# Performance work log

Measured on AMD Instinct MI355X. Metric: run time of the kernel, lower is better.

The kernel has to match this reference:

```python
import jax, jax.numpy as jnp
import numpy as np

D_MODEL = 512
N_HEADS = 8
D_K = D_MODEL // N_HEADS
LN_EPS = 1e-5


def setup_inputs() -> dict:
    key = jax.random.key(0)
    ks = jax.random.split(key, 12)
    B, S = 2, 2048
    sc = 1.0 / np.sqrt(D_MODEL)
    inp = {
        'q': jax.random.normal(ks[0], (B, S, D_MODEL), jnp.float32),
        'k': jax.random.normal(ks[1], (B, S, D_MODEL), jnp.float32),
        'v': jax.random.normal(ks[2], (B, S, D_MODEL), jnp.float32),
        'Wq': jax.random.normal(ks[3], (D_MODEL, D_MODEL), jnp.float32) * sc,
        'bq': jnp.zeros((D_MODEL,), jnp.float32),
        'Wk': jax.random.normal(ks[4], (D_MODEL, D_MODEL), jnp.float32) * sc,
        'bk': jnp.zeros((D_MODEL,), jnp.float32),
        'Wv': jax.random.normal(ks[5], (D_MODEL, D_MODEL), jnp.float32) * sc,
        'bv': jnp.zeros((D_MODEL,), jnp.float32),
        'Wo': jax.random.normal(ks[6], (D_MODEL, D_MODEL), jnp.float32) * sc,
        'bo': jnp.zeros((D_MODEL,), jnp.float32),
        'gamma': jnp.ones((D_MODEL,), jnp.float32),
        'beta': jnp.zeros((D_MODEL,), jnp.float32),
    }
    return inp


def _split_heads(x):
    B, S, _ = x.shape
    return x.reshape(B, S, N_HEADS, D_K).transpose(0, 2, 1, 3)  # [B,H,S,d_k]


def reference(q, k, v, Wq, bq, Wk, bk, Wv, bv, Wo, bo, gamma, beta):
    B, S, _ = q.shape
    Q = _split_heads(q @ Wq.T + bq)
    K = _split_heads(k @ Wk.T + bk)
    V = _split_heads(v @ Wv.T + bv)
    scores = jnp.einsum('bhqd,bhkd->bhqk', Q, K) / jnp.sqrt(jnp.float32(D_K))
    attn = jax.nn.softmax(scores, axis=-1)  # [B,H,S,S]
    out = jnp.einsum('bhqk,bhkd->bhqd', attn, V)
    out = out.transpose(0, 2, 1, 3).reshape(B, S, D_MODEL)
    out = out @ Wo.T + bo
    x = out + q  # residual
    mu = jnp.mean(x, axis=-1, keepdims=True)
    var = jnp.mean(jnp.square(x - mu), axis=-1, keepdims=True)
    y = (x - mu) * jax.lax.rsqrt(var + LN_EPS) * gamma + beta
    return (y, attn)
```

## Files before the change

### kernel.cpp

```cpp
#include <hip/hip_runtime.h>
#include <hip/hip_bf16.h>

typedef __attribute__((ext_vector_type(8))) short short8;
typedef __attribute__((ext_vector_type(4))) short short4v;
typedef __attribute__((ext_vector_type(4))) float f32x4;

#define MFMA16(A, B, C) __builtin_amdgcn_mfma_f32_16x16x32_bf16(A, B, C, 0, 0, 0)

#define SEQ 2048
#define DM 512
#define NH 8
#define DK 64
#define NROWS 4096
#define DSPLIT 4
#define ASPLIT 4
#define NT_D (SEQ / DSPLIT / 64)
#define NT_A (SEQ / ASPLIT / 64)
#define C1 0.180336880f

__device__ __forceinline__ short f2bf(float f) {
  union { float f; unsigned u; } x; x.f = f;
  unsigned r = (x.u + 0x7fffu + ((x.u >> 16) & 1u)) >> 16;
  return (short)r;
}
__device__ __forceinline__ float bf2f(short s) {
  union { unsigned u; float f; } x; x.u = ((unsigned)(unsigned short)s) << 16;
  return x.f;
}

__global__ __launch_bounds__(256) void cast_all_kernel(
    const float* __restrict__ q, const float* __restrict__ k, const float* __restrict__ v,
    const float* __restrict__ Wq, const float* __restrict__ Wk,
    const float* __restrict__ Wv, const float* __restrict__ Wo,
    short* __restrict__ qb, short* __restrict__ kb, short* __restrict__ vb,
    short* __restrict__ Wqb, short* __restrict__ Wkb,
    short* __restrict__ Wvb, short* __restrict__ Wob)
{
  int z = blockIdx.z;
  if (z >= 3 && blockIdx.x >= 128) return;
  const float* src;
  short* dst;
  switch (z) {
    case 0: src = q;  dst = qb;  break;
    case 1: src = k;  dst = kb;  break;
    case 2: src = v;  dst = vb;  break;
    case 3: src = Wq; dst = Wqb; break;
    case 4: src = Wk; dst = Wkb; break;
    case 5: src = Wv; dst = Wvb; break;
    default: src = Wo; dst = Wob; break;
  }
  size_t i = ((size_t)blockIdx.x * 256 + threadIdx.x) * 8;
  float4 f0 = *(const float4*)(src + i);
  float4 f1 = *(const float4*)(src + i + 4);
  short8 s;
  s[0] = f2bf(f0.x); s[1] = f2bf(f0.y); s[2] = f2bf(f0.z); s[3] = f2bf(f0.w);
  s[4] = f2bf(f1.x); s[5] = f2bf(f1.y); s[6] = f2bf(f1.z); s[7] = f2bf(f1.w);
  *(short8*)(dst + i) = s;
}

__global__ __launch_bounds__(256) void qkv_proj_kernel(
    const short* __restrict__ qbf, const short* __restrict__ kbf, const short* __restrict__ vbf,
    const short* __restrict__ Wqb, const short* __restrict__ Wkb, const short* __restrict__ Wvb,
    const float* __restrict__ bq, const float* __restrict__ bk, const float* __restrict__ bv,
    short* __restrict__ Qb, short* __restrict__ Kb, short* __restrict__ Vtb)
{
  int z = blockIdx.z;
  const short* X    = (z == 0) ? qbf : (z == 1) ? kbf : vbf;
  const short* W    = (z == 0) ? Wqb : (z == 1) ? Wkb : Wvb;
  const float* bias = (z == 0) ? bq  : (z == 1) ? bk  : bv;

  __shared__ short As[64][40];
  __shared__ short Bs[64][40];

  int t = threadIdx.x;
  int lane = t & 63, wave = t >> 6;
  int wr = wave >> 1, wc = wave & 1;
  int fr = lane & 15, fg = lane >> 4;
  int m0 = blockIdx.x * 64, n0 = blockIdx.y * 64;
  int lrow = t >> 2, lcol = (t & 3) * 8;

  f32x4 acc[2][2] = {};

  short8 a_pf = *(const short8*)(X + (size_t)(m0 + lrow) * DM + lcol);
  short8 b_pf = *(const short8*)(W + (size_t)(n0 + lrow) * DM + lcol);

  for (int k0 = 0; k0 < DM; k0 += 32) {
    __syncthreads();
    *(short8*)&As[lrow][lcol] = a_pf;
    *(short8*)&Bs[lrow][lcol] = b_pf;
    __syncthreads();
    if (k0 + 32 < DM) {
      a_pf = *(const short8*)(X + (size_t)(m0 + lrow) * DM + k0 + 32 + lcol);
      b_pf = *(const short8*)(W + (size_t)(n0 + lrow) * DM + k0 + 32 + lcol);
    }
    short8 a0 = *(const short8*)&As[wr * 32 + fr][fg * 8];
    short8 a1 = *(const short8*)&As[wr * 32 + 16 + fr][fg * 8];
    short8 b0 = *(const short8*)&Bs[wc * 32 + fr][fg * 8];
    short8 b1 = *(const short8*)&Bs[wc * 32 + 16 + fr][fg * 8];
    acc[0][0] = MFMA16(a0, b0, acc[0][0]);
    acc[0][1] = MFMA16(a0, b1, acc[0][1]);
    acc[1][0] = MFMA16(a1, b0, acc[1][0]);
    acc[1][1] = MFMA16(a1, b1, acc[1][1]);
  }

#pragma unroll
  for (int mi = 0; mi < 2; mi++)
#pragma unroll
    for (int ni = 0; ni < 2; ni++)
#pragma unroll
      for (int r = 0; r < 4; r++) {
        int row = m0 + wr * 32 + mi * 16 + fg * 4 + r;
        int col = n0 + wc * 32 + ni * 16 + fr;
        float val = acc[mi][ni][r] + bias[col];
        int bb = row >> 11, s = row & 2047, h = col >> 6, dk = col & 63;
        short o = f2bf(val);
        if (z == 0)      Qb[((size_t)(bb * NH + h) * SEQ + s) * DK + dk] = o;
        else if (z == 1) Kb[((size_t)(bb * NH + h) * SEQ + s) * DK + dk] = o;
        else             Vtb[((size_t)(bb * NH + h) * DK + dk) * SEQ + s] = o;
      }
}

__global__ __launch_bounds__(256) void den_kernel(
    const short* __restrict__ Q, const short* __restrict__ K, float* __restrict__ dp)
{
  __shared__ short Ks[64][72];

  int t = threadIdx.x, lane = t & 63, wave = t >> 6;
  int fr = lane & 15, fg = lane >> 4;
  int bh = blockIdx.y, z = blockIdx.z;
  const short* Qh = Q + (size_t)bh * SEQ * DK;
  const short* Kh = K + (size_t)bh * SEQ * DK;
  int q0 = blockIdx.x * 64 + wave * 16;
  const int kbase = z * (SEQ / DSPLIT);

  short8 qa0 = *(const short8*)(Qh + (q0 + fr) * DK + fg * 8);
  short8 qa1 = *(const short8*)(Qh + (q0 + fr) * DK + 32 + fg * 8);

  int r_st = t >> 2, c_st = (t & 3) * 16;

  const short* kp0 = Kh + (size_t)(kbase + r_st) * DK + c_st;
  short8 k_pf0 = *(const short8*)kp0;
  short8 k_pf1 = *(const short8*)(kp0 + 8);

  float esum = 0.f;

  for (int kt = 0; kt < NT_D; kt++) {
    __syncthreads();
    *(short8*)&Ks[r_st][c_st]     = k_pf0;
    *(short8*)&Ks[r_st][c_st + 8] = k_pf1;
    __syncthreads();
    if (kt + 1 < NT_D) {
      const short* kp = Kh + (size_t)(kbase + (kt + 1) * 64 + r_st) * DK + c_st;
      k_pf0 = *(const short8*)kp;
      k_pf1 = *(const short8*)(kp + 8);
    }
#pragma unroll
    for (int ct = 0; ct < 4; ct++) {
      short8 k0v = *(const short8*)&Ks[ct * 16 + fr][fg * 8];
      short8 k1v = *(const short8*)&Ks[ct * 16 + fr][32 + fg * 8];
      f32x4 zz = {0.f, 0.f, 0.f, 0.f};
      zz = MFMA16(k0v, qa0, zz);
      zz = MFMA16(k1v, qa1, zz);
#pragma unroll
      for (int r = 0; r < 4; r++)
        esum += __builtin_amdgcn_exp2f(zz[r] * C1);
    }
  }

  esum += __shfl_xor(esum, 16);
  esum += __shfl_xor(esum, 32);
  if (lane < 16)
    dp[((size_t)z * 16 + bh) * SEQ + q0 + lane] = esum;
}

__global__ __launch_bounds__(512) void attn_pv_kernel(
    const short* __restrict__ Q, const short* __restrict__ K, const short* __restrict__ Vt,
    const float* __restrict__ dp, float* __restrict__ attn,
    short* __restrict__ ctxp0, short* __restrict__ ctxp3)
{
  __shared__ short Ks[64][72];
  __shared__ short Vs[64][72];
  __shared__ short P[8][16][72];

  int t = threadIdx.x, lane = t & 63, wave = t >> 6;
  int fr = lane & 15, fg = lane >> 4;
  int bh = blockIdx.y, z = blockIdx.z;
  const short* Qh = Q + (size_t)bh * SEQ * DK;
  const short* Kh = K + (size_t)bh * SEQ * DK;
  const short* Vh = Vt + (size_t)bh * DK * SEQ;
  int q0 = blockIdx.x * 128 + wave * 16;
  const int kbase = z * (SEQ / ASPLIT);

  short8 qa0 = *(const short8*)(Qh + (q0 + fr) * DK + fg * 8);
  short8 qa1 = *(const short8*)(Qh + (q0 + fr) * DK + 32 + fg * 8);

  float dsum = 0.f;
#pragma unroll
  for (int zz = 0; zz < DSPLIT; zz++)
    dsum += dp[((size_t)zz * 16 + bh) * SEQ + q0 + fr];
  float lg2r = -__builtin_amdgcn_logf(dsum);

  int r_st = t >> 3, c_st = (t & 7) * 8;
  int rlo = lane >> 4, c4 = (lane & 15) * 4;

  f32x4 oacc[4] = {};

  const short* kp0 = Kh + (size_t)(kbase + r_st) * DK + c_st;
  const short* vp0 = Vh + (size_t)r_st * SEQ + kbase + c_st;
  short8 k_pf = *(const short8*)kp0;
  short8 v_pf = *(const short8*)vp0;

  for (int kt = 0; kt < NT_A; kt++) {
    int kb = kbase + kt * 64;
    __syncthreads();
    *(short8*)&Ks[r_st][c_st] = k_pf;
    *(short8*)&Vs[r_st][c_st] = v_pf;
    __syncthreads();
    if (kt + 1 < NT_A) {
      k_pf = *(const short8*)(Kh + (size_t)(kb + 64 + r_st) * DK + c_st);
      v_pf = *(const short8*)(Vh + (size_t)r_st * SEQ + kb + 64 + c_st);
    }

#pragma unroll
    for (int ct = 0; ct < 4; ct++) {
      short8 k0v = *(const short8*)&Ks[ct * 16 + fr][fg * 8];
      short8 k1v = *(const short8*)&Ks[ct * 16 + fr][32 + fg * 8];
      f32x4 zz = {0.f, 0.f, 0.f, 0.f};
      zz = MFMA16(k0v, qa0, zz);
      zz = MFMA16(k1v, qa1, zz);
      short4v pk;
#pragma unroll
      for (int r = 0; r < 4; r++)
        pk[r] = f2bf(__builtin_amdgcn_exp2f(zz[r] * C1 + lg2r));
      *(short4v*)&P[wave][fr][ct * 16 + fg * 4] = pk;
    }
    asm volatile("s_waitcnt lgkmcnt(0)" ::: "memory");

#pragma unroll
    for (int jr = 0; jr < 4; jr++) {
      int row = jr * 4 + rlo;
      short4v pv4 = *(const short4v*)&P[wave][row][c4];
      f32x4 vv = {bf2f(pv4[0]), bf2f(pv4[1]), bf2f(pv4[2]), bf2f(pv4[3])};
      *(f32x4*)&attn[((size_t)(bh * SEQ + q0 + row)) * SEQ + kb + c4] = vv;
    }

    short8 pa0 = *(const short8*)&P[wave][fr][fg * 8];
    short8 pa1 = *(const short8*)&P[wave][fr][32 + fg * 8];
#pragma unroll
    for (int dt = 0; dt < 4; dt++) {
      short8 v0 = *(const short8*)&Vs[dt * 16 + fr][fg * 8];
      short8 v1 = *(const short8*)&Vs[dt * 16 + fr][32 + fg * 8];
      oacc[dt] = MFMA16(pa0, v0, oacc[dt]);
      oacc[dt] = MFMA16(pa1, v1, oacc[dt]);
    }
  }

  int b = bh >> 3, h = bh & 7;
  short* cbase = (z < 3) ? (ctxp0 + (size_t)z * NROWS * DM) : ctxp3;
#pragma unroll
  for (int dt = 0; dt < 4; dt++)
#pragma unroll
    for (int r = 0; r < 4; r++) {
      int row = q0 + fg * 4 + r;
      cbase[((size_t)b * SEQ + row) * DM + h * 64 + dt * 16 + fr] = f2bf(oacc[dt][r]);
    }
}

__global__ __launch_bounds__(256) void oproj_kernel(
    const short* __restrict__ ctxp0, const short* __restrict__ ctxp3,
    const short* __restrict__ Wob,
    const float* __restrict__ bias, const float* __restrict__ resid,
    float* __restrict__ xout)
{
  const size_t NPART = (size_t)NROWS * DM;
  __shared__ short As[64][40];
  __shared__ short Bs[64][40];

  int t = threadIdx.x;
  int lane = t & 63, wave = t >> 6;
  int wr = wave >> 1, wc = wave & 1;
  int fr = lane & 15, fg = lane >> 4;
  int m0 = blockIdx.x * 64, n0 = blockIdx.y * 64;
  int lrow = t >> 2, lcol = (t & 3) * 8;

  f32x4 acc[2][2] = {};

  size_t ia0 = (size_t)(m0 + lrow) * DM + lcol;
  short8 a_pf0 = *(const short8*)(ctxp0 + ia0);
  short8 a_pf1 = *(const short8*)(ctxp0 + NPART + ia0);
  short8 a_pf2 = *(const short8*)(ctxp0 + 2 * NPART + ia0);
  short8 a_pf3 = *(const short8*)(ctxp3 + ia0);
  short8 b_pf = *(const short8*)(Wob + (size_t)(n0 + lrow) * DM + lcol);

  for (int k0 = 0; k0 < DM; k0 += 32) {
    __syncthreads();
    {
      short8 sv;
#pragma unroll
      for (int j = 0; j < 8; j++)
        sv[j] = f2bf(bf2f(a_pf0[j]) + bf2f(a_pf1[j]) + bf2f(a_pf2[j]) + bf2f(a_pf3[j]));
      *(short8*)&As[lrow][lcol] = sv;
      *(short8*)&Bs[lrow][lcol] = b_pf;
    }
    __syncthreads();
    if (k0 + 32 < DM) {
      size_t ia = (size_t)(m0 + lrow) * DM + k0 + 32 + lcol;
      a_pf0 = *(const short8*)(ctxp0 + ia);
      a_pf1 = *(const short8*)(ctxp0 + NPART + ia);
      a_pf2 = *(const short8*)(ctxp0 + 2 * NPART + ia);
      a_pf3 = *(const short8*)(ctxp3 + ia);
      b_pf = *(const short8*)(Wob + (size_t)(n0 + lrow) * DM + k0 + 32 + lcol);
    }
    short8 a0 = *(const short8*)&As[wr * 32 + fr][fg * 8];
    short8 a1 = *(const short8*)&As[wr * 32 + 16 + fr][fg * 8];
    short8 b0 = *(const short8*)&Bs[wc * 32 + fr][fg * 8];
    short8 b1 = *(const short8*)&Bs[wc * 32 + 16 + fr][fg * 8];
    acc[0][0] = MFMA16(a0, b0, acc[0][0]);
    acc[0][1] = MFMA16(a0, b1, acc[0][1]);
    acc[1][0] = MFMA16(a1, b0, acc[1][0]);
    acc[1][1] = MFMA16(a1, b1, acc[1][1]);
  }

#pragma unroll
  for (int mi = 0; mi < 2; mi++)
#pragma unroll
    for (int ni = 0; ni < 2; ni++)
#pragma unroll
      for (int r = 0; r < 4; r++) {
        int row = m0 + wr * 32 + mi * 16 + fg * 4 + r;
        int col = n0 + wc * 32 + ni * 16 + fr;
        float val = acc[mi][ni][r] + bias[col] + resid[(size_t)row * DM + col];
        xout[(size_t)row * DM + col] = val;
      }
}

__global__ __launch_bounds__(256) void ln_kernel(
    const float* __restrict__ x, const float* __restrict__ gamma,
    const float* __restrict__ beta, float* __restrict__ y)
{
  int row = blockIdx.x * 4 + (threadIdx.x >> 6);
  int lane = threadIdx.x & 63;
  const float4* xr = (const float4*)(x + (size_t)row * DM);
  float4 v0 = xr[lane * 2];
  float4 v1 = xr[lane * 2 + 1];
  float s = v0.x + v0.y + v0.z + v0.w + v1.x + v1.y + v1.z + v1.w;
#pragma unroll
  for (int off = 1; off < 64; off <<= 1) s += __shfl_xor(s, off);
  float mean = s * (1.0f / DM);
  float a0 = v0.x - mean, a1 = v0.y - mean, a2 = v0.z - mean, a3 = v0.w - mean;
  float a4 = v1.x - mean, a5 = v1.y - mean, a6 = v1.z - mean, a7 = v1.w - mean;
  float vs = a0 * a0 + a1 * a1 + a2 * a2 + a3 * a3 + a4 * a4 + a5 * a5 + a6 * a6 + a7 * a7;
#pragma unroll
  for (int off = 1; off < 64; off <<= 1) vs += __shfl_xor(vs, off);
  float rstd = rsqrtf(vs * (1.0f / DM) + 1e-5f);
  const float4* gp = (const float4*)gamma;
  const float4* bp = (const float4*)beta;
  float4 g0 = gp[lane * 2], g1 = gp[lane * 2 + 1];
  float4 b0 = bp[lane * 2], b1 = bp[lane * 2 + 1];
  float4 o0, o1;
  o0.x = a0 * rstd * g0.x + b0.x; o0.y = a1 * rstd * g0.y + b0.y;
  o0.z = a2 * rstd * g0.z + b0.z; o0.w = a3 * rstd * g0.w + b0.w;
  o1.x = a4 * rstd * g1.x + b1.x; o1.y = a5 * rstd * g1.y + b1.y;
  o1.z = a6 * rstd * g1.z + b1.z; o1.w = a7 * rstd * g1.w + b1.w;
  float4* yr = (float4*)(y + (size_t)row * DM);
  yr[lane * 2] = o0;
  yr[lane * 2 + 1] = o1;
}

extern "C" void kernel_launch(void* const* d_in, const int* in_sizes, int n_in,
                              void* d_out, int out_size, void* d_ws, size_t ws_size,
                              hipStream_t stream)
{
  const float* q     = (const float*)d_in[0];
  const float* k     = (const float*)d_in[1];
  const float* v     = (const float*)d_in[2];
  const float* Wq    = (const float*)d_in[3];
  const float* bq    = (const float*)d_in[4];
  const float* Wk    = (const float*)d_in[5];
  const float* bk    = (const float*)d_in[6];
  const float* Wv    = (const float*)d_in[7];
  const float* bv    = (const float*)d_in[8];
  const float* Wo    = (const float*)d_in[9];
  const float* bo    = (const float*)d_in[10];
  const float* gamma = (const float*)d_in[11];
  const float* beta  = (const float*)d_in[12];

  char* w = (char*)d_ws;
  short* qbf  = (short*)(w);
  short* kbf  = (short*)(w + ((size_t)4  << 20));
  short* vbf  = (short*)(w + ((size_t)8  << 20));
  short* Qb   = (short*)(w + ((size_t)12 << 20));
  short* Kb   = (short*)(w + ((size_t)16 << 20));
  short* Vtb  = (short*)(w + ((size_t)20 << 20));
  short* Wqb  = (short*)(w + ((size_t)24 << 20));
  short* Wkb  = (short*)(w + ((size_t)24 << 20) + ((size_t)512 << 10));
  short* Wvb  = (short*)(w + ((size_t)25 << 20));
  short* Wob  = (short*)(w + ((size_t)25 << 20) + ((size_t)512 << 10));
  float* denp = (float*)(w + ((size_t)26 << 20));
  short* ctxp0 = (short*)(w);
  short* ctxp3 = (short*)(w + ((size_t)27 << 20));
  float* xbuf  = (float*)(w + ((size_t)12 << 20));

  float* y = (float*)d_out;
  float* attnp = y + (size_t)NROWS * DM;

  cast_all_kernel<<<dim3(1024, 1, 7), 256, 0, stream>>>(q, k, v, Wq, Wk, Wv, Wo,
                                                        qbf, kbf, vbf, Wqb, Wkb, Wvb, Wob);
  qkv_proj_kernel<<<dim3(64, 8, 3), 256, 0, stream>>>(qbf, kbf, vbf, Wqb, Wkb, Wvb,
                                                      bq, bk, bv, Qb, Kb, Vtb);
  den_kernel<<<dim3(32, 16, DSPLIT), 256, 0, stream>>>(Qb, Kb, denp);
  attn_pv_kernel<<<dim3(16, 16, ASPLIT), 512, 0, stream>>>(Qb, Kb, Vtb, denp, attnp,
                                                           ctxp0, ctxp3);
  oproj_kernel<<<dim3(64, 8), 256, 0, stream>>>(ctxp0, ctxp3, Wob, bo, q, xbuf);
  ln_kernel<<<1024, 256, 0, stream>>>(xbuf, gamma, beta, y);
}
```

Before: 131.0 us.

## Enlarge QKV projection tiles to 128x128 and load via direct global-to-LDS

The QKV projection GEMM moves from 64x64 to 128x128 block tiles, so each wave computes a 4x4 grid of MFMA tiles and operands are reused more from LDS. Tile loads now use global_load_lds to write straight into shared memory instead of staging through registers with a software prefetch. The grid shrinks from 1536 to 384 blocks, which may underfill the GPU's CUs. The LDS padding is dropped, which risks bank conflicts, and the register-level prefetch overlap is lost.

```diff
diff --git a/kernel.cpp b/kernel.cpp
--- a/kernel.cpp
+++ b/kernel.cpp
@@ -26,6 +26,13 @@
 __device__ __forceinline__ float bf2f(short s) {
   union { unsigned u; float f; } x; x.u = ((unsigned)(unsigned short)s) << 16;
   return x.f;
+}
+
+__device__ __forceinline__ void gload_lds16(const short* g, short* l) {
+  __builtin_amdgcn_global_load_lds(
+      (const __attribute__((address_space(1))) void*)g,
+      (__attribute__((address_space(3))) void*)l,
+      16, 0, 0);
 }
 
 __global__ __launch_bounds__(256) void cast_all_kernel(
@@ -69,55 +76,64 @@
   const short* W    = (z == 0) ? Wqb : (z == 1) ? Wkb : Wvb;
   const float* bias = (z == 0) ? bq  : (z == 1) ? bk  : bv;
 
-  __shared__ short As[64][40];
-  __shared__ short Bs[64][40];
+  __shared__ short As[128][32];
+  __shared__ short Bs[128][32];
 
   int t = threadIdx.x;
   int lane = t & 63, wave = t >> 6;
   int wr = wave >> 1, wc = wave & 1;
   int fr = lane & 15, fg = lane >> 4;
-  int m0 = blockIdx.x * 64, n0 = blockIdx.y * 64;
-  int lrow = t >> 2, lcol = (t & 3) * 8;
-
-  f32x4 acc[2][2] = {};
-
-  short8 a_pf = *(const short8*)(X + (size_t)(m0 + lrow) * DM + lcol);
-  short8 b_pf = *(const short8*)(W + (size_t)(n0 + lrow) * DM + lcol);
+  int m0 = blockIdx.x * 128, n0 = blockIdx.y * 128;
+
+  int srow = lane >> 2, scol = (lane & 3) * 8;
+
+  f32x4 acc[4][4] = {};
 
   for (int k0 = 0; k0 < DM; k0 += 32) {
     __syncthreads();
-    *(short8*)&As[lrow][lcol] = a_pf;
-    *(short8*)&Bs[lrow][lcol] = b_pf;
-    __syncthreads();
-    if (k0 + 32 < DM) {
-      a_pf = *(const short8*)(X + (size_t)(m0 + lrow) * DM + k0 + 32 + lcol);
-      b_pf = *(const short8*)(W + (size_t)(n0 + lrow) * DM + k0 + 32 + lcol);
-    }
-    short8 a0 = *(const short8*)&As[wr * 32 + fr][fg * 8];
-    short8 a1 = *(const short8*)&As[wr * 32 + 16 + fr][fg * 8];
-    short8 b0 = *(const short8*)&Bs[wc * 32 + fr][fg * 8];
-    short8 b1 = *(const short8*)&Bs[wc * 32 + 16 + fr][fg * 8];
-    acc[0][0] = MFMA16(a0, b0, acc[0][0]);
-    acc[0][1] = MFMA16(a0, b1, acc[0][1]);
-    acc[1][0] = MFMA16(a1, b0, acc[1][0]);
-    acc[1][1] = MFMA16(a1, b1, acc[1][1]);
-  }
-
-#pragma unroll
-  for (int mi = 0; mi < 2; mi++)
-#pragma unroll
-    for (int ni = 0; ni < 2; ni++)
+    {
+      int rbase = wave * 32;
+#pragma unroll
+      for (int i = 0; i < 2; i++) {
+        const short* ga = X + (size_t)(m0 + rbase + i * 16 + srow) * DM + k0 + scol;
+        gload_lds16(ga, &As[rbase + i * 16][0]);
+        const short* gb = W + (size_t)(n0 + rbase + i * 16 + srow) * DM + k0 + scol;
+        gload_lds16(gb, &Bs[rbase + i * 16][0]);
+      }
+    }
+    __syncthreads();
+
+    short8 af[4], bf[4];
+#pragma unroll
+    for (int mi = 0; mi < 4; mi++)
+      af[mi] = *(const short8*)&As[wr * 64 + mi * 16 + fr][fg * 8];
+#pragma unroll
+    for (int ni = 0; ni < 4; ni++)
+      bf[ni] = *(const short8*)&Bs[wc * 64 + ni * 16 + fr][fg * 8];
+#pragma unroll
+    for (int mi = 0; mi < 4; mi++)
+#pragma unroll
+      for (int ni = 0; ni < 4; ni++)
+        acc[mi][ni] = MFMA16(af[mi], bf[ni], acc[mi][ni]);
+  }
+
+#pragma unroll
+  for (int ni = 0; ni < 4; ni++) {
+    int col = n0 + wc * 64 + ni * 16 + fr;
+    float bval = bias[col];
+    int h = col >> 6, dk = col & 63;
+#pragma unroll
+    for (int mi = 0; mi < 4; mi++)
 #pragma unroll
       for (int r = 0; r < 4; r++) {
-        int row = m0 + wr * 32 + mi * 16 + fg * 4 + r;
-        int col = n0 + wc * 32 + ni * 16 + fr;
-        float val = acc[mi][ni][r] + bias[col];
-        int bb = row >> 11, s = row & 2047, h = col >> 6, dk = col & 63;
-        short o = f2bf(val);
+        int row = m0 + wr * 64 + mi * 16 + fg * 4 + r;
+        int bb = row >> 11, s = row & 2047;
+        short o = f2bf(acc[mi][ni][r] + bval);
         if (z == 0)      Qb[((size_t)(bb * NH + h) * SEQ + s) * DK + dk] = o;
         else if (z == 1) Kb[((size_t)(bb * NH + h) * SEQ + s) * DK + dk] = o;
         else             Vtb[((size_t)(bb * NH + h) * DK + dk) * SEQ + s] = o;
       }
+  }
 }
 
 __global__ __launch_bounds__(256) void den_kernel(
@@ -406,7 +422,7 @@
 
   cast_all_kernel<<<dim3(1024, 1, 7), 256, 0, stream>>>(q, k, v, Wq, Wk, Wv, Wo,
                                                         qbf, kbf, vbf, Wqb, Wkb, Wvb, Wob);
-  qkv_proj_kernel<<<dim3(64, 8, 3), 256, 0, stream>>>(qbf, kbf, vbf, Wqb, Wkb, Wvb,
+  qkv_proj_kernel<<<dim3(32, 4, 3), 256, 0, stream>>>(qbf, kbf, vbf, Wqb, Wkb, Wvb,
                                                       bq, bk, bv, Qb, Kb, Vtb);
   den_kernel<<<dim3(32, 16, DSPLIT), 256, 0, stream>>>(Qb, Kb, denp);
   attn_pv_kernel<<<dim3(16, 16, ASPLIT), 512, 0, stream>>>(Qb, Kb, Vtb, denp, attnp,
```

Result: no change. 131.2 us (+0.2%).
